# Performance work log

Measured on AMD Instinct MI355X. Metric: run time of the kernel, lower is better.

The kernel has to match this reference:

```python
import jax, jax.numpy as jnp
import numpy as np


def _binarize(x):
    # sign-binarization with straight-through estimator (matches torch .data trick)
    return x + jax.lax.stop_gradient(jnp.sign(x) - x)


def _conv(x, w):
    # x: NCHW, w: OIHW, stride 1, no padding (padding handled explicitly)
    return jax.lax.conv_general_dilated(
        x, w, window_strides=(1, 1), padding='VALID',
        dimension_numbers=('NCHW', 'OIHW', 'NCHW'))


def _hardtanh(x):
    return jnp.clip(x, -1.0, 1.0)


def _maxpool2(x):
    # 2x2 max pool, stride 2, over spatial dims of NCHW
    return jax.lax.reduce_window(
        x, -jnp.inf, jax.lax.max,
        window_dimensions=(1, 1, 2, 2), window_strides=(1, 1, 2, 2),
        padding='VALID')


def setup_inputs() -> dict:
    key = jax.random.key(0)
    kx, k1, k2, k3, k4 = jax.random.split(key, 5)
    x = jax.random.normal(kx, (32, 3, 512, 512), dtype=jnp.float32)
    w1 = jax.random.normal(k1, (8, 3, 3, 3), dtype=jnp.float32) * 0.1
    w2 = jax.random.normal(k2, (16, 8, 3, 3), dtype=jnp.float32) * 0.1
    w3 = jax.random.normal(k3, (32, 16, 3, 3), dtype=jnp.float32) * 0.1
    w4 = jax.random.normal(k4, (2, 32, 3, 3), dtype=jnp.float32) * 0.1
    return {'x': x, 'w1': w1, 'w2': w2, 'w3': w3, 'w4': w4}


def reference(x, w1, w2, w3, w4):
    # p0: ConstantPad2d(1, value=1)
    h = jnp.pad(x, ((0, 0), (0, 0), (1, 1), (1, 1)), constant_values=1.0)
    # features1: BinarizeConv2d(3,8) -- input has 3 channels so NOT binarized;
    # weights are sign-binarized. Then Hardtanh, MaxPool2d(2,2).
    h = _maxpool2(_hardtanh(_conv(h, _binarize(w1))))          # [B,8,256,256]
    # features2..4: binarize activations (C != 3) and weights, conv, hardtanh
    h = _hardtanh(_conv(_binarize(h), _binarize(w2)))          # [B,16,254,254]
    h = _hardtanh(_conv(_binarize(h), _binarize(w3)))          # [B,32,252,252]
    h = _hardtanh(_conv(_binarize(h), _binarize(w4)))          # [B,2,250,250]
    return h.reshape(h.shape[0], -1)                           # [B, 125000]
```

## Files before the change

### kernel.cpp

```cpp
#include <hip/hip_runtime.h>
#include <hip/hip_bf16.h>
#include <cstdint>


typedef __attribute__((ext_vector_type(2)))  float f32x2;
typedef __attribute__((ext_vector_type(4)))  int int4v;
typedef __attribute__((ext_vector_type(16))) int int16v;

#define WOFF_W2M 0
#define WOFF_W3M 10240
#define WOFF_W4P 20480
#define WOFF_W1D 28672
#define WEIGHTS_BYTES 32768

#define A1_PB (2*256*256*4)
#define A2_PB (4*254*254*4)
#define A3_PB (8*252*252*4)

__device__ __forceinline__ int dot4(int a, int b, int c) {
#if __has_builtin(__builtin_amdgcn_sdot4)
    return __builtin_amdgcn_sdot4(a, b, c, false);
#else
    int s = c;
#pragma unroll
    for (int j = 0; j < 4; ++j) {
        int av = (a << (24 - 8 * j)) >> 24;
        int bv = (b << (24 - 8 * j)) >> 24;
        s += av * bv;
    }
    return s;
#endif
}

__device__ __forceinline__ int fsign(float w) {
    return (w > 0.f) ? 1 : ((w < 0.f) ? -1 : 0);
}

__device__ __forceinline__ void pkfma_lo(f32x2& acc, f32x2 w, f32x2 v) {
    asm("v_pk_fma_f32 %0, %1, %2, %0 op_sel:[0,0,0] op_sel_hi:[1,0,1]"
        : "+v"(acc) : "s"(w), "v"(v));
}
__device__ __forceinline__ void pkfma_hi(f32x2& acc, f32x2 w, f32x2 v) {
    asm("v_pk_fma_f32 %0, %1, %2, %0 op_sel:[0,1,0] op_sel_hi:[1,1,1]"
        : "+v"(acc) : "s"(w), "v"(v));
}

__global__ __launch_bounds__(256) void kprep(const float* __restrict__ w1,
                                             const float* __restrict__ w2,
                                             const float* __restrict__ w3,
                                             const float* __restrict__ w4,
                                             int* __restrict__ w2m,
                                             int* __restrict__ w3m,
                                             int* __restrict__ w4p,
                                             f32x2* __restrict__ w1d) {
    int tid = threadIdx.x;
    int b = blockIdx.x;
    if (b == 0) {
        for (int idx = tid; idx < 576; idx += 256) {
            int t = idx / 64, l = idx % 64;
            int oc = l & 31, icb = (l >> 5) * 16;
            int wd[4] = {0, 0, 0, 0};
            for (int j = 0; j < 16; ++j) {
                int ic = icb + j;
                int s = (oc < 16 && ic < 8) ? fsign(w2[(oc * 8 + ic) * 9 + t]) : 0;
                wd[j >> 2] |= (s & 0xff) << (8 * (j & 3));
            }
            w2m[idx * 4 + 0] = wd[0]; w2m[idx * 4 + 1] = wd[1];
            w2m[idx * 4 + 2] = wd[2]; w2m[idx * 4 + 3] = wd[3];
        }
    } else if (b == 1) {
        for (int idx = tid; idx < 576; idx += 256) {
            int t = idx / 64, l = idx % 64;
            int oc = l & 31, icb = (l >> 5) * 16;
            int wd[4] = {0, 0, 0, 0};
            for (int j = 0; j < 16; ++j) {
                int ic = icb + j;
                int s = (ic < 16) ? fsign(w3[(oc * 16 + ic) * 9 + t]) : 0;
                wd[j >> 2] |= (s & 0xff) << (8 * (j & 3));
            }
            w3m[idx * 4 + 0] = wd[0]; w3m[idx * 4 + 1] = wd[1];
            w3m[idx * 4 + 2] = wd[2]; w3m[idx * 4 + 3] = wd[3];
        }
    } else {
        for (int idx = tid; idx < 2 * 8 * 9; idx += 256) {
            int k = idx % 9, icg = (idx / 9) % 8, oc = idx / 72;
            int pack = 0;
#pragma unroll
            for (int j = 0; j < 4; ++j)
                pack |= (fsign(w4[(oc * 32 + icg * 4 + j) * 9 + k]) & 0xff) << (8 * j);
            w4p[idx] = pack;
        }
        for (int i = tid; i < 128; i += 256) {
            int op = i / 32, t = i % 32;
            f32x2 pr = {0.f, 0.f};
            if (t < 27) {
                float wa = w1[(2 * op) * 27 + t];
                float wbv = w1[(2 * op + 1) * 27 + t];
                pr[0] = (wa > 0.f) ? 1.f : ((wa < 0.f) ? -1.f : 0.f);
                pr[1] = (wbv > 0.f) ? 1.f : ((wbv < 0.f) ? -1.f : 0.f);
            }
            w1d[i] = pr;
        }
    }
}

__global__ __launch_bounds__(128, 4) void k1(const float* __restrict__ x,
                                             const f32x2* __restrict__ w1d,
                                             uint32_t* __restrict__ a1, int n0) {
    int tx = threadIdx.x;
    int oy = blockIdx.y;
    int ln = blockIdx.z;
    const float* xn = x + (size_t)(n0 + ln) * 3 * 512 * 512;

    int iy0 = 2 * oy - 1;
    int xb  = 4 * tx;

    f32x2 P[3][4][3];

    if (oy > 0 && oy < 255 && tx > 0 && tx < 127) {
#pragma unroll
        for (int ic = 0; ic < 3; ++ic) {
            const float* xc = xn + (size_t)ic * 512 * 512;
#pragma unroll
            for (int r = 0; r < 4; ++r) {
                const float* rp = xc + (size_t)(iy0 + r) * 512 + xb;
                float  lft = rp[-1];
                float4 m   = *(const float4*)rp;
                float  rgt = rp[4];
                P[ic][r][0] = (f32x2){lft, m.x};
                P[ic][r][1] = (f32x2){m.y, m.z};
                P[ic][r][2] = (f32x2){m.w, rgt};
            }
        }
    } else {
        for (int ic = 0; ic < 3; ++ic) {
            const float* xc = xn + (size_t)ic * 512 * 512;
#pragma unroll
            for (int r = 0; r < 4; ++r) {
                int iy = iy0 + r;
                bool yok = ((unsigned)iy < 512u);
                float t[6];
#pragma unroll
                for (int c = 0; c < 6; ++c) {
                    int ix = xb - 1 + c;
                    t[c] = (yok && ((unsigned)ix < 512u))
                               ? xc[(size_t)iy * 512 + ix] : 1.0f;
                }
                P[ic][r][0] = (f32x2){t[0], t[1]};
                P[ic][r][1] = (f32x2){t[2], t[3]};
                P[ic][r][2] = (f32x2){t[4], t[5]};
            }
        }
    }

#define PKTAP(ACC, ROW, COL)                                         \
    do {                                                             \
        if (((COL) & 1) == 0) pkfma_lo(ACC, ww, P[ic][ROW][(COL) >> 1]); \
        else                  pkfma_hi(ACC, ww, P[ic][ROW][(COL) >> 1]); \
    } while (0)

    uint64_t dallA = 0, dallB = 0;
#pragma unroll 1
    for (int op = 0; op < 4; ++op) {
        const f32x2* wb = w1d + op * 32;
        f32x2 wop[27];
#pragma unroll
        for (int t = 0; t < 27; ++t) wop[t] = wb[t];

        f32x2 aA00 = {0.f, 0.f}, aA01 = {0.f, 0.f};
        f32x2 aA10 = {0.f, 0.f}, aA11 = {0.f, 0.f};
        f32x2 aB00 = {0.f, 0.f}, aB01 = {0.f, 0.f};
        f32x2 aB10 = {0.f, 0.f}, aB11 = {0.f, 0.f};
#pragma unroll
        for (int ky = 0; ky < 3; ++ky) {
#pragma unroll
            for (int kx = 0; kx < 3; ++kx) {
#pragma unroll
                for (int ic = 0; ic < 3; ++ic) {
                    f32x2 ww = wop[ic * 9 + ky * 3 + kx];
                    PKTAP(aA00, ky + 0, kx + 0);
                    PKTAP(aA01, ky + 0, kx + 1);
                    PKTAP(aA10, ky + 1, kx + 0);
                    PKTAP(aA11, ky + 1, kx + 1);
                    PKTAP(aB00, ky + 0, kx + 2);
                    PKTAP(aB01, ky + 0, kx + 3);
                    PKTAP(aB10, ky + 1, kx + 2);
                    PKTAP(aB11, ky + 1, kx + 3);
                }
            }
        }
        float mA0 = fmaxf(fmaxf(aA00[0], aA01[0]), fmaxf(aA10[0], aA11[0]));
        float mA1 = fmaxf(fmaxf(aA00[1], aA01[1]), fmaxf(aA10[1], aA11[1]));
        float mB0 = fmaxf(fmaxf(aB00[0], aB01[0]), fmaxf(aB10[0], aB11[0]));
        float mB1 = fmaxf(fmaxf(aB00[1], aB01[1]), fmaxf(aB10[1], aB11[1]));
        int sA0 = (mA0 > 0.f) ? 1 : ((mA0 < 0.f) ? -1 : 0);
        int sA1 = (mA1 > 0.f) ? 1 : ((mA1 < 0.f) ? -1 : 0);
        int sB0 = (mB0 > 0.f) ? 1 : ((mB0 < 0.f) ? -1 : 0);
        int sB1 = (mB1 > 0.f) ? 1 : ((mB1 < 0.f) ? -1 : 0);
        dallA |= (uint64_t)(uint32_t)(sA0 & 0xff) << (8 * (2 * op));
        dallA |= (uint64_t)(uint32_t)(sA1 & 0xff) << (8 * (2 * op + 1));
        dallB |= (uint64_t)(uint32_t)(sB0 & 0xff) << (8 * (2 * op));
        dallB |= (uint64_t)(uint32_t)(sB1 & 0xff) << (8 * (2 * op + 1));
    }
#undef PKTAP

    size_t base = (((size_t)ln * 2) * 256 + oy) * 256 + 2 * tx;
    uint2 v0, v1;
    v0.x = (uint32_t)dallA;         v0.y = (uint32_t)dallB;
    v1.x = (uint32_t)(dallA >> 32); v1.y = (uint32_t)(dallB >> 32);
    *(uint2*)(a1 + base)             = v0;
    *(uint2*)(a1 + base + 256 * 256) = v1;
}

template<int ICG, int INW, int OUTW, int OCGO>
__global__ __launch_bounds__(256) void kconv(const uint32_t* __restrict__ ain,
                                             const int* __restrict__ wm,
                                             uint32_t* __restrict__ aout) {
    __shared__ uint32_t stb[10][36][4];
    constexpr int LG = (ICG == 2) ? 1 : 2;
    int w    = threadIdx.x >> 6;
    int lane = threadIdx.x & 63;
    int x0 = blockIdx.x * 32;
    int y0 = blockIdx.y * 8;
    int ln = blockIdx.z;

    const int4v* wmv = (const int4v*)wm;
    int4v bfr[9];
#pragma unroll
    for (int t = 0; t < 9; ++t) bfr[t] = wmv[t * 64 + lane];

    const uint32_t* abase = ain + (size_t)ln * ICG * INW * INW;
    for (int idx = threadIdx.x; idx < 10 * 36 * ICG; idx += 256) {
        int icg = idx & (ICG - 1);
        int r2 = idx >> LG;
        int xx = r2 % 36, row = r2 / 36;
        int gy = y0 + row, gx = x0 + xx;
        uint32_t val = 0;
        if (xx < 34 && gx < INW && gy < INW)
            val = abase[((size_t)icg * INW + gy) * INW + gx];
        stb[row][xx][icg] = val;
    }
    __syncthreads();

    int xl = lane & 31;
    int h  = lane >> 5;

#pragma unroll
    for (int ry = 0; ry < 2; ++ry) {
        int yy = y0 + 2 * w + ry;
        int16v acc = {};
#pragma unroll
        for (int ky = 0; ky < 3; ++ky) {
#pragma unroll
            for (int kx = 0; kx < 3; ++kx) {
                int4v a = *(const int4v*)&stb[2 * w + ry + ky][xl + kx][0];
                acc = __builtin_amdgcn_mfma_i32_32x32x32_i8(bfr[ky * 3 + kx], a, acc, 0, 0, 0);
            }
        }
        bool ok = (yy < OUTW) && (x0 + xl < OUTW);
#pragma unroll
        for (int g = 0; g < 4; ++g) {
            int ocg = 2 * g + h;
            if (ocg < OCGO && ok) {
                uint32_t dw = 0;
#pragma unroll
                for (int j = 0; j < 4; ++j) {
                    int v = min(max(acc[4 * g + j], -1), 1);
                    dw |= (uint32_t)(v & 0xff) << (8 * j);
                }
                aout[(((size_t)ln * OCGO + ocg) * OUTW + yy) * OUTW + x0 + xl] = dw;
            }
        }
    }
}

__global__ __launch_bounds__(128) void k4(const uint32_t* __restrict__ a3,
                                          const int* __restrict__ w4p,
                                          float* __restrict__ out, int n0) {
    int ox = threadIdx.x; if (ox >= 125) return;
    int oy0 = blockIdx.y * 2;
    int ln = blockIdx.z;

    int acc[2][2][2] = {};
#pragma unroll
    for (int icg = 0; icg < 8; ++icg) {
        uint32_t r[4][4];
        const uint32_t* base = a3 + (((size_t)ln * 8 + icg) * 252 + oy0) * 252 + 2 * ox;
#pragma unroll
        for (int j = 0; j < 4; ++j) {
            uint2 lo = *(const uint2*)(base + (size_t)j * 252);
            uint2 hi = *(const uint2*)(base + (size_t)j * 252 + 2);
            r[j][0] = lo.x; r[j][1] = lo.y; r[j][2] = hi.x; r[j][3] = hi.y;
        }
#pragma unroll
        for (int o = 0; o < 2; ++o) {
            const int* wb = w4p + ((o * 8 + icg) * 9);
#pragma unroll
            for (int ky = 0; ky < 3; ++ky) {
#pragma unroll
                for (int p = 0; p < 2; ++p) {
#pragma unroll
                    for (int q = 0; q < 2; ++q) {
                        acc[p][q][o] = dot4((int)r[p + ky][q + 0], wb[ky * 3 + 0], acc[p][q][o]);
                        acc[p][q][o] = dot4((int)r[p + ky][q + 1], wb[ky * 3 + 1], acc[p][q][o]);
                        acc[p][q][o] = dot4((int)r[p + ky][q + 2], wb[ky * 3 + 2], acc[p][q][o]);
                    }
                }
            }
        }
    }
    size_t gn = (size_t)(n0 + ln);
#pragma unroll
    for (int o = 0; o < 2; ++o)
#pragma unroll
        for (int p = 0; p < 2; ++p) {
            float2 w;
            w.x = fminf(fmaxf((float)acc[p][0][o], -1.f), 1.f);
            w.y = fminf(fmaxf((float)acc[p][1][o], -1.f), 1.f);
            *(float2*)(out + ((gn * 2 + o) * 250 + (oy0 + p)) * 250 + 2 * ox) = w;
        }
}

extern "C" void kernel_launch(void* const* d_in, const int* in_sizes, int n_in,
                              void* d_out, int out_size, void* d_ws, size_t ws_size,
                              hipStream_t stream) {
    const float* x  = (const float*)d_in[0];
    const float* w1 = (const float*)d_in[1];
    const float* w2 = (const float*)d_in[2];
    const float* w3 = (const float*)d_in[3];
    const float* w4 = (const float*)d_in[4];
    char* ws = (char*)d_ws;

    int*   w2m = (int*)(ws + WOFF_W2M);
    int*   w3m = (int*)(ws + WOFF_W3M);
    int*   w4p = (int*)(ws + WOFF_W4P);
    f32x2* w1d = (f32x2*)(ws + WOFF_W1D);
    float* out = (float*)d_out;

    size_t per = (size_t)A1_PB + (size_t)A2_PB + (size_t)A3_PB;
    int NC = 32;
    while (NC > 1 && (size_t)WEIGHTS_BYTES + (size_t)NC * per > ws_size) NC >>= 1;

    uint32_t* A1 = (uint32_t*)(ws + WEIGHTS_BYTES);
    uint32_t* A2 = (uint32_t*)(ws + WEIGHTS_BYTES + (size_t)NC * A1_PB);
    uint32_t* A3 = (uint32_t*)(ws + WEIGHTS_BYTES + (size_t)NC * (A1_PB + A2_PB));

    kprep<<<dim3(3), 256, 0, stream>>>(w1, w2, w3, w4, w2m, w3m, w4p, w1d);
    for (int n0 = 0; n0 < 32; n0 += NC) {
        k1<<<dim3(1, 256, NC), 128, 0, stream>>>(x, w1d, A1, n0);
        kconv<2, 256, 254, 4><<<dim3(8, 32, NC), 256, 0, stream>>>(A1, w2m, A2);
        kconv<4, 254, 252, 8><<<dim3(8, 32, NC), 256, 0, stream>>>(A2, w3m, A3);
        k4<<<dim3(1, 125, NC), 128, 0, stream>>>(A3, w4p, out, n0);
    }
}
```

Before: 150.5 us.

## Fuse conv3 and conv4 into one kernel via shared-memory tile of layer-3 output

Merges the layer-3 MFMA conv and the layer-4 dot4 conv into a single kernel. The 10x64 layer-3 tile is computed into shared memory, and layer 4 reads it from there, so the A3 global buffer and one launch are removed. The layer-3 output is recomputed at the 2-row/2-col halos between tiles. The conv2 kernel is specialised to two input channel groups and feeds zeros into the upper half of the MFMA operand instead of reading padding from LDS.

```diff
diff --git a/kernel.cpp b/kernel.cpp
--- a/kernel.cpp
+++ b/kernel.cpp
@@ -15,7 +15,6 @@
 
 #define A1_PB (2*256*256*4)
 #define A2_PB (4*254*254*4)
-#define A3_PB (8*252*252*4)
 
 __device__ __forceinline__ int dot4(int a, int b, int c) {
 #if __has_builtin(__builtin_amdgcn_sdot4)
@@ -212,12 +211,10 @@
     *(uint2*)(a1 + base + 256 * 256) = v1;
 }
 
-template<int ICG, int INW, int OUTW, int OCGO>
-__global__ __launch_bounds__(256) void kconv(const uint32_t* __restrict__ ain,
-                                             const int* __restrict__ wm,
-                                             uint32_t* __restrict__ aout) {
-    __shared__ uint32_t stb[10][36][4];
-    constexpr int LG = (ICG == 2) ? 1 : 2;
+__global__ __launch_bounds__(256) void kconv2(const uint32_t* __restrict__ ain,
+                                              const int* __restrict__ wm,
+                                              uint32_t* __restrict__ aout) {
+    __shared__ uint32_t stb[10][36][2];
     int w    = threadIdx.x >> 6;
     int lane = threadIdx.x & 63;
     int x0 = blockIdx.x * 32;
@@ -229,15 +226,15 @@
 #pragma unroll
     for (int t = 0; t < 9; ++t) bfr[t] = wmv[t * 64 + lane];
 
-    const uint32_t* abase = ain + (size_t)ln * ICG * INW * INW;
-    for (int idx = threadIdx.x; idx < 10 * 36 * ICG; idx += 256) {
-        int icg = idx & (ICG - 1);
-        int r2 = idx >> LG;
+    const uint32_t* abase = ain + (size_t)ln * 2 * 256 * 256;
+    for (int idx = threadIdx.x; idx < 10 * 36 * 2; idx += 256) {
+        int icg = idx & 1;
+        int r2 = idx >> 1;
         int xx = r2 % 36, row = r2 / 36;
         int gy = y0 + row, gx = x0 + xx;
         uint32_t val = 0;
-        if (xx < 34 && gx < INW && gy < INW)
-            val = abase[((size_t)icg * INW + gy) * INW + gx];
+        if (xx < 34 && gx < 256 && gy < 256)
+            val = abase[((size_t)icg * 256 + gy) * 256 + gx];
         stb[row][xx][icg] = val;
     }
     __syncthreads();
@@ -253,72 +250,127 @@
         for (int ky = 0; ky < 3; ++ky) {
 #pragma unroll
             for (int kx = 0; kx < 3; ++kx) {
-                int4v a = *(const int4v*)&stb[2 * w + ry + ky][xl + kx][0];
+                uint32_t d0 = stb[2 * w + ry + ky][xl + kx][0];
+                uint32_t d1 = stb[2 * w + ry + ky][xl + kx][1];
+                int4v a; a[0] = (int)d0; a[1] = (int)d1; a[2] = 0; a[3] = 0;
                 acc = __builtin_amdgcn_mfma_i32_32x32x32_i8(bfr[ky * 3 + kx], a, acc, 0, 0, 0);
             }
         }
-        bool ok = (yy < OUTW) && (x0 + xl < OUTW);
+        bool ok = (yy < 254) && (x0 + xl < 254);
 #pragma unroll
         for (int g = 0; g < 4; ++g) {
             int ocg = 2 * g + h;
-            if (ocg < OCGO && ok) {
+            if (ocg < 4 && ok) {
                 uint32_t dw = 0;
 #pragma unroll
                 for (int j = 0; j < 4; ++j) {
                     int v = min(max(acc[4 * g + j], -1), 1);
                     dw |= (uint32_t)(v & 0xff) << (8 * j);
                 }
-                aout[(((size_t)ln * OCGO + ocg) * OUTW + yy) * OUTW + x0 + xl] = dw;
-            }
-        }
-    }
-}
-
-__global__ __launch_bounds__(128) void k4(const uint32_t* __restrict__ a3,
-                                          const int* __restrict__ w4p,
-                                          float* __restrict__ out, int n0) {
-    int ox = threadIdx.x; if (ox >= 125) return;
-    int oy0 = blockIdx.y * 2;
+                aout[(((size_t)ln * 4 + ocg) * 254 + yy) * 254 + x0 + xl] = dw;
+            }
+        }
+    }
+}
+
+__global__ __launch_bounds__(256) void kconv34(const uint32_t* __restrict__ a2,
+                                               const int* __restrict__ w3m,
+                                               const int* __restrict__ w4p,
+                                               float* __restrict__ out, int n0) {
+    __shared__ uint32_t sA2[12][68][4];
+    __shared__ uint32_t sA3[10][8][64];
+    int w    = threadIdx.x >> 6;
+    int lane = threadIdx.x & 63;
+    int x0 = blockIdx.x * 50;
+    int y0 = blockIdx.y * 8;
     int ln = blockIdx.z;
 
-    int acc[2][2][2] = {};
-#pragma unroll
-    for (int icg = 0; icg < 8; ++icg) {
-        uint32_t r[4][4];
-        const uint32_t* base = a3 + (((size_t)ln * 8 + icg) * 252 + oy0) * 252 + 2 * ox;
-#pragma unroll
-        for (int j = 0; j < 4; ++j) {
-            uint2 lo = *(const uint2*)(base + (size_t)j * 252);
-            uint2 hi = *(const uint2*)(base + (size_t)j * 252 + 2);
-            r[j][0] = lo.x; r[j][1] = lo.y; r[j][2] = hi.x; r[j][3] = hi.y;
-        }
-#pragma unroll
-        for (int o = 0; o < 2; ++o) {
-            const int* wb = w4p + ((o * 8 + icg) * 9);
-#pragma unroll
-            for (int ky = 0; ky < 3; ++ky) {
-#pragma unroll
-                for (int p = 0; p < 2; ++p) {
-#pragma unroll
-                    for (int q = 0; q < 2; ++q) {
-                        acc[p][q][o] = dot4((int)r[p + ky][q + 0], wb[ky * 3 + 0], acc[p][q][o]);
-                        acc[p][q][o] = dot4((int)r[p + ky][q + 1], wb[ky * 3 + 1], acc[p][q][o]);
-                        acc[p][q][o] = dot4((int)r[p + ky][q + 2], wb[ky * 3 + 2], acc[p][q][o]);
-                    }
+    const int4v* wmv = (const int4v*)w3m;
+    int4v bfr[9];
+#pragma unroll
+    for (int t = 0; t < 9; ++t) bfr[t] = wmv[t * 64 + lane];
+
+    const uint32_t* abase = a2 + (size_t)ln * 4 * 254 * 254;
+    for (int idx = threadIdx.x; idx < 12 * 66 * 4; idx += 256) {
+        int icg = idx & 3;
+        int r2 = idx >> 2;
+        int xx = r2 % 66, row = r2 / 66;
+        int gy = y0 + row, gx = x0 + xx;
+        uint32_t val = 0;
+        if (gy < 254 && gx < 254)
+            val = abase[((size_t)icg * 254 + gy) * 254 + gx];
+        sA2[row][xx][icg] = val;
+    }
+    __syncthreads();
+
+    int xl = lane & 31;
+    int h  = lane >> 5;
+#pragma unroll
+    for (int t5 = 0; t5 < 5; ++t5) {
+        int t = w * 5 + t5;
+        int ct = t / 10, row = t % 10;
+        int16v acc = {};
+#pragma unroll
+        for (int ky = 0; ky < 3; ++ky) {
+#pragma unroll
+            for (int kx = 0; kx < 3; ++kx) {
+                int4v a = *(const int4v*)&sA2[row + ky][ct * 32 + xl + kx][0];
+                acc = __builtin_amdgcn_mfma_i32_32x32x32_i8(bfr[ky * 3 + kx], a, acc, 0, 0, 0);
+            }
+        }
+#pragma unroll
+        for (int g = 0; g < 4; ++g) {
+            uint32_t dw = 0;
+#pragma unroll
+            for (int j = 0; j < 4; ++j) {
+                int v = min(max(acc[4 * g + j], -1), 1);
+                dw |= (uint32_t)(v & 0xff) << (8 * j);
+            }
+            sA3[row][2 * g + h][ct * 32 + xl] = dw;
+        }
+    }
+    __syncthreads();
+
+    size_t gn = (size_t)(n0 + ln);
+    int o = threadIdx.x;
+    if (o < 200) {
+        int y  = o / 25;
+        int xp = (o % 25) * 2;
+        int gy = y0 + y;
+        if (gy < 250) {
+            int acc00 = 0, acc01 = 0, acc10 = 0, acc11 = 0;
+#pragma unroll
+            for (int icg = 0; icg < 8; ++icg) {
+#pragma unroll
+                for (int ky = 0; ky < 3; ++ky) {
+                    uint2 lo = *(const uint2*)&sA3[y + ky][icg][xp];
+                    uint2 hi = *(const uint2*)&sA3[y + ky][icg][xp + 2];
+                    int c0 = (int)lo.x, c1 = (int)lo.y, c2 = (int)hi.x, c3 = (int)hi.y;
+                    const int* wb0 = w4p + (0 * 8 + icg) * 9 + ky * 3;
+                    const int* wb1 = w4p + (1 * 8 + icg) * 9 + ky * 3;
+                    acc00 = dot4(c0, wb0[0], acc00);
+                    acc00 = dot4(c1, wb0[1], acc00);
+                    acc00 = dot4(c2, wb0[2], acc00);
+                    acc01 = dot4(c0, wb1[0], acc01);
+                    acc01 = dot4(c1, wb1[1], acc01);
+                    acc01 = dot4(c2, wb1[2], acc01);
+                    acc10 = dot4(c1, wb0[0], acc10);
+                    acc10 = dot4(c2, wb0[1], acc10);
+                    acc10 = dot4(c3, wb0[2], acc10);
+                    acc11 = dot4(c1, wb1[0], acc11);
+                    acc11 = dot4(c2, wb1[1], acc11);
+                    acc11 = dot4(c3, wb1[2], acc11);
                 }
             }
-        }
-    }
-    size_t gn = (size_t)(n0 + ln);
-#pragma unroll
-    for (int o = 0; o < 2; ++o)
-#pragma unroll
-        for (int p = 0; p < 2; ++p) {
-            float2 w;
-            w.x = fminf(fmaxf((float)acc[p][0][o], -1.f), 1.f);
-            w.y = fminf(fmaxf((float)acc[p][1][o], -1.f), 1.f);
-            *(float2*)(out + ((gn * 2 + o) * 250 + (oy0 + p)) * 250 + 2 * ox) = w;
-        }
+            float2 o0, o1;
+            o0.x = fminf(fmaxf((float)acc00, -1.f), 1.f);
+            o0.y = fminf(fmaxf((float)acc10, -1.f), 1.f);
+            o1.x = fminf(fmaxf((float)acc01, -1.f), 1.f);
+            o1.y = fminf(fmaxf((float)acc11, -1.f), 1.f);
+            *(float2*)(out + ((gn * 2 + 0) * 250 + gy) * 250 + x0 + xp) = o0;
+            *(float2*)(out + ((gn * 2 + 1) * 250 + gy) * 250 + x0 + xp) = o1;
+        }
+    }
 }
 
 extern "C" void kernel_launch(void* const* d_in, const int* in_sizes, int n_in,
@@ -337,19 +389,17 @@
     f32x2* w1d = (f32x2*)(ws + WOFF_W1D);
     float* out = (float*)d_out;
 
-    size_t per = (size_t)A1_PB + (size_t)A2_PB + (size_t)A3_PB;
+    size_t per = (size_t)A1_PB + (size_t)A2_PB;
     int NC = 32;
     while (NC > 1 && (size_t)WEIGHTS_BYTES + (size_t)NC * per > ws_size) NC >>= 1;
 
     uint32_t* A1 = (uint32_t*)(ws + WEIGHTS_BYTES);
     uint32_t* A2 = (uint32_t*)(ws + WEIGHTS_BYTES + (size_t)NC * A1_PB);
-    uint32_t* A3 = (uint32_t*)(ws + WEIGHTS_BYTES + (size_t)NC * (A1_PB + A2_PB));
 
     kprep<<<dim3(3), 256, 0, stream>>>(w1, w2, w3, w4, w2m, w3m, w4p, w1d);
     for (int n0 = 0; n0 < 32; n0 += NC) {
         k1<<<dim3(1, 256, NC), 128, 0, stream>>>(x, w1d, A1, n0);
-        kconv<2, 256, 254, 4><<<dim3(8, 32, NC), 256, 0, stream>>>(A1, w2m, A2);
-        kconv<4, 254, 252, 8><<<dim3(8, 32, NC), 256, 0, stream>>>(A2, w3m, A3);
-        k4<<<dim3(1, 125, NC), 128, 0, stream>>>(A3, w4p, out, n0);
-    }
-}
+        kconv2<<<dim3(8, 32, NC), 256, 0, stream>>>(A1, w2m, A2);
+        kconv34<<<dim3(5, 32, NC), 256, 0, stream>>>(A2, w3m, w4p, out, n0);
+    }
+}
```

New measurement: 146.0 us. -3.0%, faster.
